# Optimization experiments

Hardware: AMD Instinct MI355X
Metric: run time of the kernel (lower is better)

Reference implementation:

```python
import jax, jax.numpy as jnp
import numpy as np

DIM = 1024          # moe_cfg.dim
INTER = 1024        # moe_cfg.moe_inter_dim
E = 8               # moe_cfg.n_routed_experts
TOPK = 2            # moe_cfg.n_activated_experts
ROUTE_SCALE = 1.0
SHARED_INTER = 2048 # n_shared_experts * moe_inter_dim
B, S = 4, 2048


def setup_inputs() -> dict:
    key = jax.random.key(0)
    ks = jax.random.split(key, 10)
    def w(k, shape, scale=0.02):
        return jax.random.normal(k, shape, jnp.float32) * scale
    return {
        "x": jax.random.normal(ks[0], (B, S, DIM), jnp.float32),
        # Gate (nn.Linear(dim, n_routed_experts, bias=True))
        "gate_w": w(ks[1], (E, DIM)),
        "gate_b": jnp.zeros((E,), jnp.float32),
        # Routed experts, stacked on leading E axis (torch Linear convention: [out, in])
        "w1": w(ks[2], (E, INTER, DIM)), "b1": jnp.zeros((E, INTER), jnp.float32),
        "w3": w(ks[3], (E, INTER, DIM)), "b3": jnp.zeros((E, INTER), jnp.float32),
        "w2": w(ks[4], (E, DIM, INTER)), "b2": jnp.zeros((E, DIM), jnp.float32),
        # Shared expert MLP(dim, n_shared_experts * moe_inter_dim)
        "ws1": w(ks[5], (SHARED_INTER, DIM)), "bs1": jnp.zeros((SHARED_INTER,), jnp.float32),
        "ws3": w(ks[6], (SHARED_INTER, DIM)), "bs3": jnp.zeros((SHARED_INTER,), jnp.float32),
        "ws2": w(ks[7], (DIM, SHARED_INTER)), "bs2": jnp.zeros((DIM,), jnp.float32),
    }


def _moe_forward(x, gate_w, gate_b, w1, b1, w3, b3, w2, b2,
                 ws1, bs1, ws3, bs3, ws2, bs2):
    Bq, Sq, D = x.shape
    xt = x.reshape(-1, D)  # [T, D], T = B*S
    # ---- Gate: softmax scores in fp32, top-k routing (eval mode: no usage buffers) ----
    logits = (xt @ gate_w.T + gate_b).astype(jnp.float32)  # [T, E]
    scores = jax.nn.softmax(logits, axis=-1)
    top_w, top_i = jax.lax.top_k(scores, TOPK)             # values == gathered scores
    weights = (top_w * ROUTE_SCALE).astype(x.dtype)        # [T, topk]
    # Dense combine weights [T, E]: zero for unrouted experts (math identical to dispatch)
    gate_dense = jnp.sum(jax.nn.one_hot(top_i, E, dtype=x.dtype) * weights[..., None], axis=1)
    # ---- Routed experts: SwiGLU FFN per expert (dropout p=0 -> identity) ----
    def expert(w1e, b1e, w3e, b3e, w2e, b2e):
        h = jax.nn.silu(xt @ w1e.T + b1e) * (xt @ w3e.T + b3e)  # [T, INTER]
        return h @ w2e.T + b2e                                   # [T, D]
    outs = jax.vmap(expert)(w1, b1, w3, b3, w2, b2)  # [E, T, D]
    y = jnp.einsum('etd,te->td', outs, gate_dense)   # weighted combine
    # ---- Shared expert MLP (SwiGLU) ----
    z = (jax.nn.silu(xt @ ws1.T + bs1) * (xt @ ws3.T + bs3)) @ ws2.T + bs2
    return (y + z).reshape(Bq, Sq, D)


def reference(x, gate_w, gate_b, w1, b1, w3, b3, w2, b2,
              ws1, bs1, ws3, bs3, ws2, bs2):
    return _moe_forward(x, gate_w, gate_b, w1, b1, w3, b3, w2, b2,
                        ws1, bs1, ws3, bs3, ws2, bs2)
```

## Files before the change

kernel.cpp:

```cpp
#include <hip/hip_runtime.h>
#include <stdint.h>
#include <stddef.h>

#define T_TOK  8192
#define DIMK   1024
#define INTERK 1024
#define NEXP   8
#define SINT   2048
#define CAP    18432
#define RT256  72

#define NS1_R  16
#define NS1_S  32
#define RT_S   32
#define G1R    (NS1_R * RT256)
#define G1     (G1R + NS1_S * RT_S)
#define NS2    8
#define G2R    (NS2 * RT256)
#define G2     (G2R + NS2 * RT_S)

typedef float  f32x4  __attribute__((ext_vector_type(4)));
typedef short  bf16x8 __attribute__((ext_vector_type(8)));

typedef __attribute__((address_space(1))) const unsigned int gas_u32;
typedef __attribute__((address_space(3))) unsigned int las_u32;

__device__ __forceinline__ void gload16(const void* g, void* l) {
  __builtin_amdgcn_global_load_lds((gas_u32*)g, (las_u32*)l, 16, 0, 0);
}

__device__ __forceinline__ unsigned short f2b(float f) {
  unsigned int u = __float_as_uint(f);
  u = (u + 0x7FFFu + ((u >> 16) & 1u)) >> 16;
  return (unsigned short)u;
}
__device__ __forceinline__ float b2f(unsigned short h) {
  return __uint_as_float(((unsigned int)h) << 16);
}

__device__ __forceinline__ void barrier_nodrain() {
  asm volatile("" ::: "memory");
  __builtin_amdgcn_s_barrier();
  asm volatile("" ::: "memory");
}

#define N1C 2097152
#define N2C 524288
#define N3C 2097152
#define N4C 524288
#define WCVT_BLOCKS ((2*N1C + 2*N2C + N3C + N4C) / 256)
__global__ __launch_bounds__(256) void wcvt_all_kernel(
    const float4* __restrict__ w1, const float4* __restrict__ w3,
    const float4* __restrict__ ws1, const float4* __restrict__ ws3,
    const float4* __restrict__ w2, const float4* __restrict__ ws2,
    unsigned short* __restrict__ w13r, unsigned short* __restrict__ w13s,
    unsigned short* __restrict__ w2b, unsigned short* __restrict__ ws2b) {
  long long i = (long long)blockIdx.x * 256 + threadIdx.x;
  float4 v;
  unsigned short* dst;
  size_t didx;
  if (i < 2 * (long long)N1C) {
    int is3 = i >= N1C;
    int j = (int)(i - (long long)is3 * N1C);
    int r = j >> 8, kc = j & 255;
    int e = r >> 10, rr = r & 1023, g = rr >> 4;
    size_t dst_r = (size_t)e * (2 * INTERK) + g * 32 + (is3 ? 16 : 0) + (rr & 15);
    v = (is3 ? w3 : w1)[j];
    dst = w13r; didx = dst_r * 256 + kc;
  } else if ((i -= 2 * (long long)N1C) < 2 * (long long)N2C) {
    int is3 = i >= N2C;
    int j = (int)(i - (long long)is3 * N2C);
    int r = j >> 8, kc = j & 255;
    int g = r >> 4;
    size_t dst_r = (size_t)g * 32 + (is3 ? 16 : 0) + (r & 15);
    v = (is3 ? ws3 : ws1)[j];
    dst = w13s; didx = dst_r * 256 + kc;
  } else if ((i -= 2 * (long long)N2C) < (long long)N3C) {
    int j = (int)i;
    v = w2[j];
    dst = w2b; didx = (size_t)j;
  } else {
    int j = (int)(i - N3C);
    v = ws2[j];
    dst = ws2b; didx = (size_t)j;
  }
  ushort4 o;
  o.x = f2b(v.x); o.y = f2b(v.y); o.z = f2b(v.z); o.w = f2b(v.w);
  *reinterpret_cast<ushort4*>(&dst[didx * 4]) = o;
}

__global__ __launch_bounds__(256) void gate_cvt_kernel(
    const float* __restrict__ x, const float* __restrict__ gw, const float* __restrict__ gb,
    int* __restrict__ top_i, float* __restrict__ top_w,
    unsigned short* __restrict__ xb) {
  int t    = blockIdx.x * 4 + (threadIdx.x >> 6);
  int lane = threadIdx.x & 63;
  const float* xr = x + (size_t)t * DIMK;
  unsigned short* xo = xb + (size_t)t * DIMK;
  float acc[NEXP];
#pragma unroll
  for (int e = 0; e < NEXP; ++e) acc[e] = 0.f;
  for (int i = lane; i < DIMK; i += 64) {
    float xv = xr[i];
    xo[i] = f2b(xv);
#pragma unroll
    for (int e = 0; e < NEXP; ++e) acc[e] += xv * gw[e * DIMK + i];
  }
#pragma unroll
  for (int e = 0; e < NEXP; ++e) {
    float v = acc[e];
#pragma unroll
    for (int off = 32; off > 0; off >>= 1) v += __shfl_down(v, off, 64);
    acc[e] = v;
  }
  if (lane == 0) {
    float lg[NEXP];
#pragma unroll
    for (int e = 0; e < NEXP; ++e) lg[e] = acc[e] + gb[e];
    int i0 = 0;
#pragma unroll
    for (int e = 1; e < NEXP; ++e) if (lg[e] > lg[i0]) i0 = e;
    int i1 = (i0 == 0) ? 1 : 0;
#pragma unroll
    for (int e = 0; e < NEXP; ++e) if (e != i0 && lg[e] > lg[i1]) i1 = e;
    float mx = lg[i0], s = 0.f;
#pragma unroll
    for (int e = 0; e < NEXP; ++e) s += expf(lg[e] - mx);
    top_i[t * 2]     = i0;
    top_i[t * 2 + 1] = i1;
    top_w[t * 2]     = expf(lg[i0] - mx) / s;
    top_w[t * 2 + 1] = expf(lg[i1] - mx) / s;
  }
}

__global__ __launch_bounds__(512) void route_build_kernel(
    const int* __restrict__ top_i, int* __restrict__ order, int* __restrict__ pos,
    int* __restrict__ poff_g) {
  __shared__ int cnt[NEXP][512];
  __shared__ int base[NEXP][512];
  __shared__ int totals[NEXP];
  __shared__ int poff_s[NEXP + 1];
  int tid = threadIdx.x;
  int lane = tid & 63, w = tid >> 6;
  const int t0 = tid * 16;

  int c[NEXP];
#pragma unroll
  for (int e = 0; e < NEXP; ++e) c[e] = 0;
  for (int j = 0; j < 16; ++j) {
    int e0 = top_i[(t0 + j) * 2];
    int e1 = top_i[(t0 + j) * 2 + 1];
#pragma unroll
    for (int e = 0; e < NEXP; ++e) c[e] += (e0 == e) + (e1 == e);
  }
#pragma unroll
  for (int e = 0; e < NEXP; ++e) cnt[e][tid] = c[e];
  __syncthreads();

  {
    int running = 0;
    for (int ch = 0; ch < 8; ++ch) {
      int v = cnt[w][ch * 64 + lane];
      int incl = v;
#pragma unroll
      for (int off = 1; off < 64; off <<= 1) {
        int u = __shfl_up(incl, off, 64);
        if (lane >= off) incl += u;
      }
      base[w][ch * 64 + lane] = running + incl - v;
      running += __shfl(incl, 63, 64);
    }
    if (lane == 0) totals[w] = running;
  }
  __syncthreads();

  if (tid == 0) {
    int off = 0;
#pragma unroll
    for (int e = 0; e < NEXP; ++e) {
      poff_s[e] = off;
      off += (totals[e] + 255) & ~255;
    }
    poff_s[NEXP] = off;
#pragma unroll
    for (int e = 0; e <= NEXP; ++e) poff_g[e] = poff_s[e];
  }
  __syncthreads();

  int cur[NEXP];
#pragma unroll
  for (int e = 0; e < NEXP; ++e) cur[e] = poff_s[e] + base[e][tid];
  for (int j = 0; j < 16; ++j) {
    int t = t0 + j;
#pragma unroll
    for (int k = 0; k < 2; ++k) {
      int ei = top_i[t * 2 + k];
      int p = 0;
#pragma unroll
      for (int e = 0; e < NEXP; ++e)
        if (ei == e) { p = cur[e]; cur[e] = p + 1; }
      order[p]       = t;
      pos[t * 2 + k] = p;
    }
  }

#pragma unroll
  for (int e = 0; e < NEXP; ++e) {
    int s = poff_s[e] + totals[e], en = poff_s[e + 1];
    for (int i = s + tid; i < en; i += 512) order[i] = 0;
  }
}

#define A_ELE   16384
#define B_ELE   8192
#define BUF_ELE (A_ELE + B_ELE)

template <bool SWIGLU>
__device__ __forceinline__ void gemm_core(
    const unsigned short* __restrict__ A, int lda, int K,
    const int* __restrict__ order, bool gather, int rowbase,
    const unsigned short* __restrict__ Be,
    const float* __restrict__ bias1e, const float* __restrict__ bias3e,
    int ncolbase, void* __restrict__ outp, int ldo, bool outf32,
    unsigned short* lds) {
  int tid = threadIdx.x;
  int lane = tid & 63, wid = tid >> 6;
  int wr = wid >> 1, wc = wid & 1;

  size_t aoff[4], boff[2];
#pragma unroll
  for (int l = 0; l < 4; ++l) {
    int g = l * 512 + tid;
    int r = g >> 3;
    int sub = (g & 7) ^ (r & 7);
    int gr = gather ? order[rowbase + r] : (rowbase + r);
    aoff[l] = (size_t)gr * lda + (size_t)(sub * 8);
  }
#pragma unroll
  for (int l = 0; l < 2; ++l) {
    int g = l * 512 + tid;
    int r = g >> 3;
    int sub = (g & 7) ^ (r & 7);
    boff[l] = (size_t)(ncolbase + r) * K + (size_t)(sub * 8);
  }

  f32x4 acc[4][4];
#pragma unroll
  for (int m = 0; m < 4; ++m)
#pragma unroll
    for (int n = 0; n < 4; ++n) acc[m][n] = f32x4{0.f, 0.f, 0.f, 0.f};

  const int NT = K >> 6;

#pragma unroll
  for (int l = 0; l < 4; ++l)
    gload16(A + aoff[l], &lds[(size_t)(l * 512 + tid) * 8]);
#pragma unroll
  for (int l = 0; l < 2; ++l)
    gload16(Be + boff[l], &lds[A_ELE + (size_t)(l * 512 + tid) * 8]);
#pragma unroll
  for (int l = 0; l < 4; ++l)
    gload16(A + aoff[l] + 64, &lds[BUF_ELE + (size_t)(l * 512 + tid) * 8]);
#pragma unroll
  for (int l = 0; l < 2; ++l)
    gload16(Be + boff[l] + 64, &lds[BUF_ELE + A_ELE + (size_t)(l * 512 + tid) * 8]);

  unsigned int off_r = 0, off_m = BUF_ELE, off_w = 2 * BUF_ELE;

  for (int t = 0; t < NT; ++t) {
    if (t + 1 < NT) {
      asm volatile("s_waitcnt vmcnt(6)" ::: "memory");
    } else {
      asm volatile("s_waitcnt vmcnt(0)" ::: "memory");
    }
    asm volatile("s_waitcnt lgkmcnt(0)" ::: "memory");
    barrier_nodrain();

    const unsigned short* Ab = &lds[off_r];
    const unsigned short* Bb = &lds[off_r + A_ELE];
    const bool st = (t + 2 < NT);
    const int kb = (t + 2) << 6;

    {
      bf16x8 a[4], b[4];
#pragma unroll
      for (int m = 0; m < 4; ++m) {
        int ra = wr * 64 + m * 16 + (lane & 15);
        int sa = ((lane >> 4)) ^ (ra & 7);
        a[m] = *(const bf16x8*)&Ab[ra * 64 + sa * 8];
      }
#pragma unroll
      for (int n = 0; n < 4; ++n) {
        int rb = wc * 64 + n * 16 + (lane & 15);
        int sb = ((lane >> 4)) ^ (rb & 7);
        b[n] = *(const bf16x8*)&Bb[rb * 64 + sb * 8];
      }
      if (st) {
#pragma unroll
        for (int l = 0; l < 4; ++l)
          gload16(A + aoff[l] + kb, &lds[off_w + (size_t)(l * 512 + tid) * 8]);
      }
      __builtin_amdgcn_s_setprio(1);
#pragma unroll
      for (int m = 0; m < 4; ++m)
#pragma unroll
        for (int n = 0; n < 4; ++n)
          acc[m][n] = __builtin_amdgcn_mfma_f32_16x16x32_bf16(a[m], b[n], acc[m][n], 0, 0, 0);
      __builtin_amdgcn_s_setprio(0);
    }
    {
      bf16x8 a[4], b[4];
#pragma unroll
      for (int m = 0; m < 4; ++m) {
        int ra = wr * 64 + m * 16 + (lane & 15);
        int sa = (4 + (lane >> 4)) ^ (ra & 7);
        a[m] = *(const bf16x8*)&Ab[ra * 64 + sa * 8];
      }
#pragma unroll
      for (int n = 0; n < 4; ++n) {
        int rb = wc * 64 + n * 16 + (lane & 15);
        int sb = (4 + (lane >> 4)) ^ (rb & 7);
        b[n] = *(const bf16x8*)&Bb[rb * 64 + sb * 8];
      }
      if (st) {
#pragma unroll
        for (int l = 0; l < 2; ++l)
          gload16(Be + boff[l] + kb, &lds[off_w + A_ELE + (size_t)(l * 512 + tid) * 8]);
      }
      __builtin_amdgcn_s_setprio(1);
#pragma unroll
      for (int m = 0; m < 4; ++m)
#pragma unroll
        for (int n = 0; n < 4; ++n)
          acc[m][n] = __builtin_amdgcn_mfma_f32_16x16x32_bf16(a[m], b[n], acc[m][n], 0, 0, 0);
      __builtin_amdgcn_s_setprio(0);
    }

    unsigned int tmp = off_r; off_r = off_m; off_m = off_w; off_w = tmp;
  }

  if (SWIGLU) {
#pragma unroll
    for (int m = 0; m < 4; ++m)
#pragma unroll
      for (int np = 0; np < 2; ++np) {
        int realcol = (ncolbase >> 1) + wc * 32 + np * 16 + (lane & 15);
        float bb1 = bias1e[realcol];
        float bb3 = bias3e[realcol];
#pragma unroll
        for (int j = 0; j < 4; ++j) {
          int row  = rowbase + wr * 64 + m * 16 + (lane >> 4) * 4 + j;
          float a1 = acc[m][2 * np][j] + bb1;
          float a3 = acc[m][2 * np + 1][j] + bb3;
          float hv = (a1 / (1.f + __expf(-a1))) * a3;
          ((unsigned short*)outp)[(size_t)row * ldo + realcol] = f2b(hv);
        }
      }
  } else {
#pragma unroll
    for (int m = 0; m < 4; ++m)
#pragma unroll
      for (int n = 0; n < 4; ++n) {
        int col  = ncolbase + wc * 64 + n * 16 + (lane & 15);
        float bb = bias1e[col];
#pragma unroll
        for (int j = 0; j < 4; ++j) {
          int row = rowbase + wr * 64 + m * 16 + (lane >> 4) * 4 + j;
          float v = acc[m][n][j] + bb;
          if (outf32)
            ((float*)outp)[(size_t)row * ldo + col] = v;
          else
            ((unsigned short*)outp)[(size_t)row * ldo + col] = f2b(v);
        }
      }
  }
}

__global__ __launch_bounds__(512) void gemm1m_kernel(
    const unsigned short* __restrict__ xb,
    const int* __restrict__ order, const int* __restrict__ poff,
    const unsigned short* __restrict__ w13r,
    const float* __restrict__ b1, const float* __restrict__ b3,
    const unsigned short* __restrict__ w13s,
    const float* __restrict__ bs1, const float* __restrict__ bs3,
    unsigned short* __restrict__ h, unsigned short* __restrict__ hs) {
  __shared__ unsigned short lds[3 * BUF_ELE];

  int raw = blockIdx.x;
  int id  = (raw & 7) * (G1 / 8) + (raw >> 3);

  if (id < G1R) {
    int by = id / NS1_R, bx = id - by * NS1_R;
    int rowbase = by * 256;
    if (rowbase >= poff[NEXP]) return;
    int expert = 0;
    while (expert < NEXP - 1 && rowbase >= poff[expert + 1]) ++expert;
    gemm_core<true>(xb, DIMK, DIMK, order, true, rowbase,
                    w13r + (size_t)expert * 2 * INTERK * DIMK,
                    b1 + expert * INTERK, b3 + expert * INTERK,
                    bx * 128, (void*)h, INTERK, false, lds);
  } else {
    int id2 = id - G1R;
    int by = id2 / NS1_S, bx = id2 - by * NS1_S;
    gemm_core<true>(xb, DIMK, DIMK, (const int*)nullptr, false, by * 256,
                    w13s, bs1, bs3,
                    bx * 128, (void*)hs, SINT, false, lds);
  }
}

__global__ __launch_bounds__(512) void gemm2m_kernel(
    const unsigned short* __restrict__ h, const unsigned short* __restrict__ hs,
    const int* __restrict__ poff,
    const unsigned short* __restrict__ w2b, const float* __restrict__ b2,
    const unsigned short* __restrict__ ws2b, const float* __restrict__ bs2,
    unsigned short* __restrict__ yb, float* __restrict__ out) {
  __shared__ unsigned short lds[3 * BUF_ELE];

  int raw = blockIdx.x;
  int id  = (raw & 7) * (G2 / 8) + (raw >> 3);

  if (id < G2R) {
    int by = id / NS2, bx = id - by * NS2;
    int rowbase = by * 256;
    if (rowbase >= poff[NEXP]) return;
    int expert = 0;
    while (expert < NEXP - 1 && rowbase >= poff[expert + 1]) ++expert;
    gemm_core<false>(h, INTERK, INTERK, (const int*)nullptr, false, rowbase,
                     w2b + (size_t)expert * DIMK * INTERK,
                     b2 + expert * DIMK, (const float*)nullptr,
                     bx * 128, (void*)yb, DIMK, false, lds);
  } else {
    int id2 = id - G2R;
    int by = id2 / NS2, bx = id2 - by * NS2;
    gemm_core<false>(hs, SINT, SINT, (const int*)nullptr, false, by * 256,
                     ws2b, bs2, (const float*)nullptr,
                     bx * 128, (void*)out, DIMK, true, lds);
  }
}

__global__ __launch_bounds__(256) void combine4_kernel(
    float* __restrict__ out, const unsigned short* __restrict__ y,
    const int* __restrict__ pos, const float* __restrict__ tw) {
  int t  = blockIdx.x;
  int d4 = threadIdx.x;
  int p0 = pos[t * 2], p1 = pos[t * 2 + 1];
  float w0 = tw[t * 2], w1 = tw[t * 2 + 1];
  ushort4 y0 = ((const ushort4*)(y + (size_t)p0 * DIMK))[d4];
  ushort4 y1 = ((const ushort4*)(y + (size_t)p1 * DIMK))[d4];
  float4* o4 = (float4*)(out + (size_t)t * DIMK);
  float4 o = o4[d4];
  o.x += w0 * b2f(y0.x) + w1 * b2f(y1.x);
  o.y += w0 * b2f(y0.y) + w1 * b2f(y1.y);
  o.z += w0 * b2f(y0.z) + w1 * b2f(y1.z);
  o.w += w0 * b2f(y0.w) + w1 * b2f(y1.w);
  o4[d4] = o;
}

extern "C" void kernel_launch(void* const* d_in, const int* in_sizes, int n_in,
                              void* d_out, int out_size, void* d_ws, size_t ws_size,
                              hipStream_t stream) {
  const float* x   = (const float*)d_in[0];
  const float* gw  = (const float*)d_in[1];
  const float* gb  = (const float*)d_in[2];
  const float* w1  = (const float*)d_in[3];
  const float* b1  = (const float*)d_in[4];
  const float* w3  = (const float*)d_in[5];
  const float* b3  = (const float*)d_in[6];
  const float* w2  = (const float*)d_in[7];
  const float* b2  = (const float*)d_in[8];
  const float* ws1 = (const float*)d_in[9];
  const float* bs1 = (const float*)d_in[10];
  const float* ws3 = (const float*)d_in[11];
  const float* bs3 = (const float*)d_in[12];
  const float* ws2 = (const float*)d_in[13];
  const float* bs2 = (const float*)d_in[14];
  float* out = (float*)d_out;
  (void)in_sizes; (void)n_in; (void)out_size; (void)ws_size;

  char* p = (char*)d_ws;
  auto alloc = [&](size_t bytes) -> void* {
    void* r = (void*)p;
    p += (bytes + 255) & ~(size_t)255;
    return r;
  };
  unsigned short* xb    = (unsigned short*)alloc((size_t)T_TOK * DIMK * 2);
  unsigned short* w13r  = (unsigned short*)alloc((size_t)NEXP * 2 * INTERK * DIMK * 2);
  unsigned short* w2b   = (unsigned short*)alloc((size_t)NEXP * DIMK * INTERK * 2);
  unsigned short* w13s  = (unsigned short*)alloc((size_t)2 * SINT * DIMK * 2);
  unsigned short* ws2b  = (unsigned short*)alloc((size_t)DIMK * SINT * 2);
  unsigned short* h     = (unsigned short*)alloc((size_t)CAP * INTERK * 2);
  unsigned short* yb    = (unsigned short*)alloc((size_t)CAP * DIMK * 2);
  unsigned short* hs    = (unsigned short*)alloc((size_t)T_TOK * SINT * 2);
  int*   top_i  = (int*)alloc((size_t)T_TOK * 2 * 4);
  float* top_w  = (float*)alloc((size_t)T_TOK * 2 * 4);
  int*   pos    = (int*)alloc((size_t)T_TOK * 2 * 4);
  int*   order  = (int*)alloc((size_t)CAP * 4);
  int*   poff   = (int*)alloc(64);

  gate_cvt_kernel<<<T_TOK / 4, 256, 0, stream>>>(x, gw, gb, top_i, top_w, xb);
  route_build_kernel<<<1, 512, 0, stream>>>(top_i, order, pos, poff);
  wcvt_all_kernel<<<WCVT_BLOCKS, 256, 0, stream>>>(
      (const float4*)w1, (const float4*)w3, (const float4*)ws1, (const float4*)ws3,
      (const float4*)w2, (const float4*)ws2, w13r, w13s, w2b, ws2b);

  gemm1m_kernel<<<G1, 512, 0, stream>>>(xb, order, poff, w13r, b1, b3,
                                        w13s, bs1, bs3, h, hs);
  gemm2m_kernel<<<G2, 512, 0, stream>>>(h, hs, poff, w2b, b2, ws2b, bs2, yb, out);

  combine4_kernel<<<T_TOK, 256, 0, stream>>>(out, yb, pos, top_w);
}
```

Measured before the change: 375.6 us.

## Fuse gate with weight conversion and scatter-add routed outputs via atomics

Gate/x-conversion and weight conversion are merged into one launch. The second GEMM is split into a shared-expert pass that writes fp32 output first, then a routed pass whose epilogue multiplies by per-slot routing weights and atomically adds into the output. This removes the bf16 yb intermediate and the separate combine kernel. The cost is scattered fp32 atomics, nondeterministic summation order, and the two GEMM2 passes now running serially instead of sharing one grid.

```diff
diff --git a/kernel.cpp b/kernel.cpp
--- a/kernel.cpp
+++ b/kernel.cpp
@@ -17,7 +17,7 @@
 #define G1     (G1R + NS1_S * RT_S)
 #define NS2    8
 #define G2R    (NS2 * RT256)
-#define G2     (G2R + NS2 * RT_S)
+#define G2S    (NS2 * RT_S)
 
 typedef float  f32x4  __attribute__((ext_vector_type(4)));
 typedef short  bf16x8 __attribute__((ext_vector_type(8)));
@@ -48,14 +48,59 @@
 #define N2C 524288
 #define N3C 2097152
 #define N4C 524288
+#define GATE_BLOCKS (T_TOK / 4)
 #define WCVT_BLOCKS ((2*N1C + 2*N2C + N3C + N4C) / 256)
-__global__ __launch_bounds__(256) void wcvt_all_kernel(
+__global__ __launch_bounds__(256) void cvtgate_kernel(
+    const float* __restrict__ x, const float* __restrict__ gw, const float* __restrict__ gb,
+    int* __restrict__ top_i, float* __restrict__ top_w, unsigned short* __restrict__ xb,
     const float4* __restrict__ w1, const float4* __restrict__ w3,
     const float4* __restrict__ ws1, const float4* __restrict__ ws3,
     const float4* __restrict__ w2, const float4* __restrict__ ws2,
     unsigned short* __restrict__ w13r, unsigned short* __restrict__ w13s,
     unsigned short* __restrict__ w2b, unsigned short* __restrict__ ws2b) {
-  long long i = (long long)blockIdx.x * 256 + threadIdx.x;
+  int bid = blockIdx.x;
+  if (bid < GATE_BLOCKS) {
+    int t    = bid * 4 + (threadIdx.x >> 6);
+    int lane = threadIdx.x & 63;
+    const float* xr = x + (size_t)t * DIMK;
+    unsigned short* xo = xb + (size_t)t * DIMK;
+    float acc[NEXP];
+#pragma unroll
+    for (int e = 0; e < NEXP; ++e) acc[e] = 0.f;
+    for (int i = lane; i < DIMK; i += 64) {
+      float xv = xr[i];
+      xo[i] = f2b(xv);
+#pragma unroll
+      for (int e = 0; e < NEXP; ++e) acc[e] += xv * gw[e * DIMK + i];
+    }
+#pragma unroll
+    for (int e = 0; e < NEXP; ++e) {
+      float v = acc[e];
+#pragma unroll
+      for (int off = 32; off > 0; off >>= 1) v += __shfl_down(v, off, 64);
+      acc[e] = v;
+    }
+    if (lane == 0) {
+      float lg[NEXP];
+#pragma unroll
+      for (int e = 0; e < NEXP; ++e) lg[e] = acc[e] + gb[e];
+      int i0 = 0;
+#pragma unroll
+      for (int e = 1; e < NEXP; ++e) if (lg[e] > lg[i0]) i0 = e;
+      int i1 = (i0 == 0) ? 1 : 0;
+#pragma unroll
+      for (int e = 0; e < NEXP; ++e) if (e != i0 && lg[e] > lg[i1]) i1 = e;
+      float mx = lg[i0], s = 0.f;
+#pragma unroll
+      for (int e = 0; e < NEXP; ++e) s += expf(lg[e] - mx);
+      top_i[t * 2]     = i0;
+      top_i[t * 2 + 1] = i1;
+      top_w[t * 2]     = expf(lg[i0] - mx) / s;
+      top_w[t * 2 + 1] = expf(lg[i1] - mx) / s;
+    }
+    return;
+  }
+  long long i = (long long)(bid - GATE_BLOCKS) * 256 + threadIdx.x;
   float4 v;
   unsigned short* dst;
   size_t didx;
@@ -89,53 +134,9 @@
   *reinterpret_cast<ushort4*>(&dst[didx * 4]) = o;
 }
 
-__global__ __launch_bounds__(256) void gate_cvt_kernel(
-    const float* __restrict__ x, const float* __restrict__ gw, const float* __restrict__ gb,
-    int* __restrict__ top_i, float* __restrict__ top_w,
-    unsigned short* __restrict__ xb) {
-  int t    = blockIdx.x * 4 + (threadIdx.x >> 6);
-  int lane = threadIdx.x & 63;
-  const float* xr = x + (size_t)t * DIMK;
-  unsigned short* xo = xb + (size_t)t * DIMK;
-  float acc[NEXP];
-#pragma unroll
-  for (int e = 0; e < NEXP; ++e) acc[e] = 0.f;
-  for (int i = lane; i < DIMK; i += 64) {
-    float xv = xr[i];
-    xo[i] = f2b(xv);
-#pragma unroll
-    for (int e = 0; e < NEXP; ++e) acc[e] += xv * gw[e * DIMK + i];
-  }
-#pragma unroll
-  for (int e = 0; e < NEXP; ++e) {
-    float v = acc[e];
-#pragma unroll
-    for (int off = 32; off > 0; off >>= 1) v += __shfl_down(v, off, 64);
-    acc[e] = v;
-  }
-  if (lane == 0) {
-    float lg[NEXP];
-#pragma unroll
-    for (int e = 0; e < NEXP; ++e) lg[e] = acc[e] + gb[e];
-    int i0 = 0;
-#pragma unroll
-    for (int e = 1; e < NEXP; ++e) if (lg[e] > lg[i0]) i0 = e;
-    int i1 = (i0 == 0) ? 1 : 0;
-#pragma unroll
-    for (int e = 0; e < NEXP; ++e) if (e != i0 && lg[e] > lg[i1]) i1 = e;
-    float mx = lg[i0], s = 0.f;
-#pragma unroll
-    for (int e = 0; e < NEXP; ++e) s += expf(lg[e] - mx);
-    top_i[t * 2]     = i0;
-    top_i[t * 2 + 1] = i1;
-    top_w[t * 2]     = expf(lg[i0] - mx) / s;
-    top_w[t * 2 + 1] = expf(lg[i1] - mx) / s;
-  }
-}
-
 __global__ __launch_bounds__(512) void route_build_kernel(
-    const int* __restrict__ top_i, int* __restrict__ order, int* __restrict__ pos,
-    int* __restrict__ poff_g) {
+    const int* __restrict__ top_i, const float* __restrict__ top_w,
+    int* __restrict__ order, float* __restrict__ wslot, int* __restrict__ poff_g) {
   __shared__ int cnt[NEXP][512];
   __shared__ int base[NEXP][512];
   __shared__ int totals[NEXP];
@@ -199,15 +200,15 @@
 #pragma unroll
       for (int e = 0; e < NEXP; ++e)
         if (ei == e) { p = cur[e]; cur[e] = p + 1; }
-      order[p]       = t;
-      pos[t * 2 + k] = p;
+      order[p] = t;
+      wslot[p] = top_w[t * 2 + k];
     }
   }
 
 #pragma unroll
   for (int e = 0; e < NEXP; ++e) {
     int s = poff_s[e] + totals[e], en = poff_s[e + 1];
-    for (int i = s + tid; i < en; i += 512) order[i] = 0;
+    for (int i = s + tid; i < en; i += 512) { order[i] = 0; wslot[i] = 0.f; }
   }
 }
 
@@ -215,13 +216,14 @@
 #define B_ELE   8192
 #define BUF_ELE (A_ELE + B_ELE)
 
-template <bool SWIGLU>
+template <int EPI>
 __device__ __forceinline__ void gemm_core(
     const unsigned short* __restrict__ A, int lda, int K,
     const int* __restrict__ order, bool gather, int rowbase,
     const unsigned short* __restrict__ Be,
     const float* __restrict__ bias1e, const float* __restrict__ bias3e,
-    int ncolbase, void* __restrict__ outp, int ldo, bool outf32,
+    int ncolbase, void* __restrict__ outp, int ldo,
+    const int* __restrict__ tokmap, const float* __restrict__ wslot,
     unsigned short* lds) {
   int tid = threadIdx.x;
   int lane = tid & 63, wid = tid >> 6;
@@ -339,7 +341,7 @@
     unsigned int tmp = off_r; off_r = off_m; off_m = off_w; off_w = tmp;
   }
 
-  if (SWIGLU) {
+  if (EPI == 0) {
 #pragma unroll
     for (int m = 0; m < 4; ++m)
 #pragma unroll
@@ -356,7 +358,7 @@
           ((unsigned short*)outp)[(size_t)row * ldo + realcol] = f2b(hv);
         }
       }
-  } else {
+  } else if (EPI == 2) {
 #pragma unroll
     for (int m = 0; m < 4; ++m)
 #pragma unroll
@@ -366,13 +368,25 @@
 #pragma unroll
         for (int j = 0; j < 4; ++j) {
           int row = rowbase + wr * 64 + m * 16 + (lane >> 4) * 4 + j;
-          float v = acc[m][n][j] + bb;
-          if (outf32)
-            ((float*)outp)[(size_t)row * ldo + col] = v;
-          else
-            ((unsigned short*)outp)[(size_t)row * ldo + col] = f2b(v);
+          ((float*)outp)[(size_t)row * ldo + col] = acc[m][n][j] + bb;
         }
       }
+  } else {
+#pragma unroll
+    for (int m = 0; m < 4; ++m) {
+#pragma unroll
+      for (int j = 0; j < 4; ++j) {
+        int row = rowbase + wr * 64 + m * 16 + (lane >> 4) * 4 + j;
+        int tok = tokmap[row];
+        float wg = wslot[row];
+#pragma unroll
+        for (int n = 0; n < 4; ++n) {
+          int col  = ncolbase + wc * 64 + n * 16 + (lane & 15);
+          float v  = wg * (acc[m][n][j] + bias1e[col]);
+          atomicAdd(&((float*)outp)[(size_t)tok * ldo + col], v);
+        }
+      }
+    }
   }
 }
 
@@ -395,65 +409,49 @@
     if (rowbase >= poff[NEXP]) return;
     int expert = 0;
     while (expert < NEXP - 1 && rowbase >= poff[expert + 1]) ++expert;
-    gemm_core<true>(xb, DIMK, DIMK, order, true, rowbase,
-                    w13r + (size_t)expert * 2 * INTERK * DIMK,
-                    b1 + expert * INTERK, b3 + expert * INTERK,
-                    bx * 128, (void*)h, INTERK, false, lds);
+    gemm_core<0>(xb, DIMK, DIMK, order, true, rowbase,
+                 w13r + (size_t)expert * 2 * INTERK * DIMK,
+                 b1 + expert * INTERK, b3 + expert * INTERK,
+                 bx * 128, (void*)h, INTERK, nullptr, nullptr, lds);
   } else {
     int id2 = id - G1R;
     int by = id2 / NS1_S, bx = id2 - by * NS1_S;
-    gemm_core<true>(xb, DIMK, DIMK, (const int*)nullptr, false, by * 256,
-                    w13s, bs1, bs3,
-                    bx * 128, (void*)hs, SINT, false, lds);
-  }
-}
-
-__global__ __launch_bounds__(512) void gemm2m_kernel(
-    const unsigned short* __restrict__ h, const unsigned short* __restrict__ hs,
-    const int* __restrict__ poff,
+    gemm_core<0>(xb, DIMK, DIMK, (const int*)nullptr, false, by * 256,
+                 w13s, bs1, bs3,
+                 bx * 128, (void*)hs, SINT, nullptr, nullptr, lds);
+  }
+}
+
+__global__ __launch_bounds__(512) void gemm2s_kernel(
+    const unsigned short* __restrict__ hs,
+    const unsigned short* __restrict__ ws2b, const float* __restrict__ bs2,
+    float* __restrict__ out) {
+  __shared__ unsigned short lds[3 * BUF_ELE];
+  int raw = blockIdx.x;
+  int id  = (raw & 7) * (G2S / 8) + (raw >> 3);
+  int by = id / NS2, bx = id - by * NS2;
+  gemm_core<2>(hs, SINT, SINT, (const int*)nullptr, false, by * 256,
+               ws2b, bs2, (const float*)nullptr,
+               bx * 128, (void*)out, DIMK, nullptr, nullptr, lds);
+}
+
+__global__ __launch_bounds__(512) void gemm2r_kernel(
+    const unsigned short* __restrict__ h, const int* __restrict__ poff,
     const unsigned short* __restrict__ w2b, const float* __restrict__ b2,
-    const unsigned short* __restrict__ ws2b, const float* __restrict__ bs2,
-    unsigned short* __restrict__ yb, float* __restrict__ out) {
+    const int* __restrict__ order, const float* __restrict__ wslot,
+    float* __restrict__ out) {
   __shared__ unsigned short lds[3 * BUF_ELE];
-
   int raw = blockIdx.x;
-  int id  = (raw & 7) * (G2 / 8) + (raw >> 3);
-
-  if (id < G2R) {
-    int by = id / NS2, bx = id - by * NS2;
-    int rowbase = by * 256;
-    if (rowbase >= poff[NEXP]) return;
-    int expert = 0;
-    while (expert < NEXP - 1 && rowbase >= poff[expert + 1]) ++expert;
-    gemm_core<false>(h, INTERK, INTERK, (const int*)nullptr, false, rowbase,
-                     w2b + (size_t)expert * DIMK * INTERK,
-                     b2 + expert * DIMK, (const float*)nullptr,
-                     bx * 128, (void*)yb, DIMK, false, lds);
-  } else {
-    int id2 = id - G2R;
-    int by = id2 / NS2, bx = id2 - by * NS2;
-    gemm_core<false>(hs, SINT, SINT, (const int*)nullptr, false, by * 256,
-                     ws2b, bs2, (const float*)nullptr,
-                     bx * 128, (void*)out, DIMK, true, lds);
-  }
-}
-
-__global__ __launch_bounds__(256) void combine4_kernel(
-    float* __restrict__ out, const unsigned short* __restrict__ y,
-    const int* __restrict__ pos, const float* __restrict__ tw) {
-  int t  = blockIdx.x;
-  int d4 = threadIdx.x;
-  int p0 = pos[t * 2], p1 = pos[t * 2 + 1];
-  float w0 = tw[t * 2], w1 = tw[t * 2 + 1];
-  ushort4 y0 = ((const ushort4*)(y + (size_t)p0 * DIMK))[d4];
-  ushort4 y1 = ((const ushort4*)(y + (size_t)p1 * DIMK))[d4];
-  float4* o4 = (float4*)(out + (size_t)t * DIMK);
-  float4 o = o4[d4];
-  o.x += w0 * b2f(y0.x) + w1 * b2f(y1.x);
-  o.y += w0 * b2f(y0.y) + w1 * b2f(y1.y);
-  o.z += w0 * b2f(y0.z) + w1 * b2f(y1.z);
-  o.w += w0 * b2f(y0.w) + w1 * b2f(y1.w);
-  o4[d4] = o;
+  int id  = (raw & 7) * (G2R / 8) + (raw >> 3);
+  int by = id / NS2, bx = id - by * NS2;
+  int rowbase = by * 256;
+  if (rowbase >= poff[NEXP]) return;
+  int expert = 0;
+  while (expert < NEXP - 1 && rowbase >= poff[expert + 1]) ++expert;
+  gemm_core<3>(h, INTERK, INTERK, (const int*)nullptr, false, rowbase,
+               w2b + (size_t)expert * DIMK * INTERK,
+               b2 + expert * DIMK, (const float*)nullptr,
+               bx * 128, (void*)out, DIMK, order, wslot, lds);
 }
 
 extern "C" void kernel_launch(void* const* d_in, const int* in_sizes, int n_in,
@@ -489,23 +487,22 @@
   unsigned short* w13s  = (unsigned short*)alloc((size_t)2 * SINT * DIMK * 2);
   unsigned short* ws2b  = (unsigned short*)alloc((size_t)DIMK * SINT * 2);
   unsigned short* h     = (unsigned short*)alloc((size_t)CAP * INTERK * 2);
-  unsigned short* yb    = (unsigned short*)alloc((size_t)CAP * DIMK * 2);
   unsigned short* hs    = (unsigned short*)alloc((size_t)T_TOK * SINT * 2);
   int*   top_i  = (int*)alloc((size_t)T_TOK * 2 * 4);
   float* top_w  = (float*)alloc((size_t)T_TOK * 2 * 4);
-  int*   pos    = (int*)alloc((size_t)T_TOK * 2 * 4);
   int*   order  = (int*)alloc((size_t)CAP * 4);
+  float* wslot  = (float*)alloc((size_t)CAP * 4);
   int*   poff   = (int*)alloc(64);
 
-  gate_cvt_kernel<<<T_TOK / 4, 256, 0, stream>>>(x, gw, gb, top_i, top_w, xb);
-  route_build_kernel<<<1, 512, 0, stream>>>(top_i, order, pos, poff);
-  wcvt_all_kernel<<<WCVT_BLOCKS, 256, 0, stream>>>(
+  cvtgate_kernel<<<GATE_BLOCKS + WCVT_BLOCKS, 256, 0, stream>>>(
+      x, gw, gb, top_i, top_w, xb,
       (const float4*)w1, (const float4*)w3, (const float4*)ws1, (const float4*)ws3,
       (const float4*)w2, (const float4*)ws2, w13r, w13s, w2b, ws2b);
+  route_build_kernel<<<1, 512, 0, stream>>>(top_i, top_w, order, wslot, poff);
 
   gemm1m_kernel<<<G1, 512, 0, stream>>>(xb, order, poff, w13r, b1, b3,
                                         w13s, bs1, bs3, h, hs);
-  gemm2m_kernel<<<G2, 512, 0, stream>>>(h, hs, poff, w2b, b2, ws2b, bs2, yb, out);
-
-  combine4_kernel<<<T_TOK, 256, 0, stream>>>(out, yb, pos, top_w);
-}
+
+  gemm2s_kernel<<<G2S, 512, 0, stream>>>(hs, ws2b, bs2, out);
+  gemm2r_kernel<<<G2R, 512, 0, stream>>>(h, poff, w2b, b2, order, wslot, out);
+}
```

New measurement: 448.7 us. +19.4%, slower.
